# Optimization experiments

Measured on AMD Instinct MI355X. Metric: run time of the kernel, lower is better.

## Reference

```python
import jax, jax.numpy as jnp
import numpy as np

N_NODES = 100000
D_IN = 256
D_OUT = 128
N_EDGES = 1600000


def setup_inputs() -> dict:
    key = jax.random.key(0)
    k1, k2, k3, k4 = jax.random.split(key, 4)
    x = jax.random.normal(k1, (N_NODES, D_IN), dtype=jnp.float32)
    edge_index = jax.random.randint(k2, (2, N_EDGES), 0, N_NODES, dtype=jnp.int64)
    # GCNConv parameters (glorot-style scale)
    W = jax.random.normal(k3, (D_IN, D_OUT), dtype=jnp.float32) * (1.0 / np.sqrt(D_IN))
    b = jax.random.normal(k4, (D_OUT,), dtype=jnp.float32) * 0.01
    return {"x": x, "edge_index": edge_index, "W": W, "b": b}


def reference(x, edge_index, W, b):
    n = x.shape[0]
    # add self-loops (PyG GCNConv default)
    loop = jnp.arange(n, dtype=edge_index.dtype)
    src = jnp.concatenate([edge_index[0], loop])
    dst = jnp.concatenate([edge_index[1], loop])
    # symmetric normalization: deg^-1/2[src] * deg^-1/2[dst]
    ones = jnp.ones(src.shape[0], dtype=x.dtype)
    deg = jax.ops.segment_sum(ones, dst, num_segments=n)
    dinv = jnp.where(deg > 0, jax.lax.rsqrt(deg), 0.0)
    norm = dinv[src] * dinv[dst]  # [E+N]
    # linear transform at nodes, then gather-scale-scatter over edges
    h = x @ W  # [N, d_out]
    msg = h[src] * norm[:, None]  # [E+N, d_out]
    out = jax.ops.segment_sum(msg, dst, num_segments=n) + b
    # CRD.forward: relu then dropout (identity in eval mode)
    return jax.nn.relu(out)
```

## Files before the change

### kernel.cpp

```cpp
#include <hip/hip_runtime.h>
#include <stdint.h>

#define D_IN 256
#define D_OUT 128
#define MAXB 800
#define NCHUNK 256

typedef __attribute__((ext_vector_type(8))) short bf16x8;
typedef __attribute__((ext_vector_type(4))) float f32x4;

__device__ __forceinline__ unsigned short f2bf(float f) {
  union { float f; uint32_t u; } v; v.f = f;
  uint32_t u = v.u;
  uint32_t r = (u + 0x7FFFu + ((u >> 16) & 1u)) >> 16;
  return (unsigned short)r;
}
__device__ __forceinline__ float bf_lo(uint32_t u) {
  union { uint32_t u; float f; } v; v.u = u << 16; return v.f;
}
__device__ __forceinline__ float bf_hi(uint32_t u) {
  union { uint32_t u; float f; } v; v.u = u & 0xFFFF0000u; return v.f;
}
__device__ __forceinline__ f32x4 bq_a(uint4 u) {
  return f32x4{bf_lo(u.x), bf_hi(u.x), bf_lo(u.y), bf_hi(u.y)};
}
__device__ __forceinline__ f32x4 bq_b(uint4 u) {
  return f32x4{bf_lo(u.z), bf_hi(u.z), bf_lo(u.w), bf_hi(u.w)};
}

__device__ __forceinline__ void dma16(const float* gsrc, float* ldst) {
  __builtin_amdgcn_global_load_lds(
      (const __attribute__((address_space(1))) void*)gsrc,
      (__attribute__((address_space(3))) void*)ldst, 16, 0, 0);
}

__global__ __launch_bounds__(256) void k_conv_w(const float* __restrict__ W,
                                                unsigned short* __restrict__ wt) {
  int idx = blockIdx.x * 256 + threadIdx.x;
  int n = idx >> 8;
  int k = idx & 255;
  wt[idx] = f2bf(W[k * D_OUT + n]);
}

__global__ __launch_bounds__(512) void k_gemm(const float* __restrict__ x,
                                              const unsigned short* __restrict__ wt,
                                              const float* __restrict__ dinv,
                                              unsigned short* __restrict__ hp, int N) {
  __shared__ float xl[2][16][256];

  int wave = threadIdx.x >> 6;
  int lane = threadIdx.x & 63;
  int m = lane & 15;
  int q = lane >> 4;

  bf16x8 bw[8];
  const unsigned short* wrow = wt + (size_t)(wave * 16 + m) * D_IN + q * 8;
#pragma unroll
  for (int kt = 0; kt < 8; ++kt)
    bw[kt] = *reinterpret_cast<const bf16x8*>(wrow + kt * 32);

  int tiles = (N + 15) >> 4;
  int ipb = (tiles + gridDim.x - 1) / gridDim.x;
  int t0 = blockIdx.x * ipb;
  int tend = t0 + ipb;
  if (tend > tiles) tend = tiles;
  if (t0 >= tend) return;

  auto stage_tile = [&](int buf, int tt) {
#pragma unroll
    for (int rr = 0; rr < 2; ++rr) {
      int r = wave + rr * 8;
      const float* gsrc = x + ((size_t)tt * 16 + r) * D_IN + ((lane ^ (r & 7)) << 2);
      dma16(gsrc, &xl[buf][r][0]);
    }
  };

  stage_tile(0, t0);
  __syncthreads();

  int cur = 0;
  int sw = m & 7;

  for (int t = t0; t < tend; ++t) {
    if (t + 1 < tend) stage_tile(cur ^ 1, t + 1);

    const float* prow = &xl[cur][m][0];
    f32x4 acc = {0.f, 0.f, 0.f, 0.f};
#pragma unroll
    for (int kt = 0; kt < 8; ++kt) {
      int g0 = q * 2 + kt * 8;
      float4 u0 = *reinterpret_cast<const float4*>(prow + ((g0 ^ sw) << 2));
      float4 u1 = *reinterpret_cast<const float4*>(prow + (((g0 + 1) ^ sw) << 2));
      bf16x8 av;
      av[0] = (short)f2bf(u0.x); av[1] = (short)f2bf(u0.y);
      av[2] = (short)f2bf(u0.z); av[3] = (short)f2bf(u0.w);
      av[4] = (short)f2bf(u1.x); av[5] = (short)f2bf(u1.y);
      av[6] = (short)f2bf(u1.z); av[7] = (short)f2bf(u1.w);
      acc = __builtin_amdgcn_mfma_f32_16x16x32_bf16(av, bw[kt], acc, 0, 0, 0);
    }

    int r0 = t * 16;
#pragma unroll
    for (int r = 0; r < 4; ++r) {
      int row = r0 + q * 4 + r;
      hp[(size_t)row * D_OUT + wave * 16 + m] = f2bf(dinv[row] * acc[r]);
    }

    __syncthreads();
    cur ^= 1;
  }
}

__global__ __launch_bounds__(256) void k_passA(const int* __restrict__ ei, int E, int CH,
                                               int NB, int* __restrict__ cntm) {
  __shared__ int bins[MAXB];
  int c = blockIdx.x;
  for (int b = threadIdx.x; b < NB; b += 256) bins[b] = 0;
  __syncthreads();
  int start = c * CH, end = min(E, start + CH);
  for (int eb = start + (int)threadIdx.x * 4; eb < end; eb += 1024) {
    int kmax = end - eb; if (kmax > 4) kmax = 4;
    if (kmax == 4) {
      int4 v = *reinterpret_cast<const int4*>(ei + E + eb);
      atomicAdd(&bins[v.x >> 7], 1);
      atomicAdd(&bins[v.y >> 7], 1);
      atomicAdd(&bins[v.z >> 7], 1);
      atomicAdd(&bins[v.w >> 7], 1);
    } else {
      for (int k = 0; k < kmax; ++k) atomicAdd(&bins[ei[E + eb + k] >> 7], 1);
    }
  }
  __syncthreads();
  for (int b = threadIdx.x; b < NB; b += 256) cntm[(size_t)b * NCHUNK + c] = bins[b];
}

__global__ __launch_bounds__(NCHUNK) void k_scanB1(const int* __restrict__ cntm,
                                                   int* __restrict__ ofs,
                                                   int* __restrict__ tot) {
  __shared__ int sc[NCHUNK];
  int b = blockIdx.x, t = threadIdx.x;
  int v = cntm[(size_t)b * NCHUNK + t];
  sc[t] = v;
  __syncthreads();
  for (int off = 1; off < NCHUNK; off <<= 1) {
    int val = (t >= off) ? sc[t - off] : 0;
    __syncthreads();
    sc[t] += val;
    __syncthreads();
  }
  ofs[(size_t)b * NCHUNK + t] = sc[t] - v;
  if (t == NCHUNK - 1) tot[b] = sc[t];
}

__global__ __launch_bounds__(256) void k_scanB2(const int* __restrict__ tot,
                                                int* __restrict__ base, int NB,
                                                int* __restrict__ nptr, int N, int E) {
  __shared__ int sc[256];
  int t = threadIdx.x;
  int v[4];
  int s = 0;
#pragma unroll
  for (int j = 0; j < 4; ++j) {
    int i = t * 4 + j;
    v[j] = (i < NB) ? tot[i] : 0;
    s += v[j];
  }
  sc[t] = s;
  __syncthreads();
  for (int off = 1; off < 256; off <<= 1) {
    int val = (t >= off) ? sc[t - off] : 0;
    __syncthreads();
    sc[t] += val;
    __syncthreads();
  }
  int ex = sc[t] - s;
#pragma unroll
  for (int j = 0; j < 4; ++j) {
    int i = t * 4 + j;
    if (i < NB) base[i] = ex;
    ex += v[j];
  }
  if (t == 0) nptr[N] = E;
}

__global__ __launch_bounds__(256) void k_passC(const int* __restrict__ ei, int E, int CH,
                                               int NB, const int* __restrict__ ofs,
                                               const int* __restrict__ base,
                                               int* __restrict__ P) {
  __shared__ int cur[MAXB];
  int c = blockIdx.x;
  for (int b = threadIdx.x; b < NB; b += 256)
    cur[b] = base[b] + ofs[(size_t)b * NCHUNK + c];
  __syncthreads();
  int start = c * CH, end = min(E, start + CH);
  for (int eb = start + (int)threadIdx.x * 4; eb < end; eb += 1024) {
    int kmax = end - eb; if (kmax > 4) kmax = 4;
    int s4[4], d4[4];
    if (kmax == 4) {
      int4 vs = *reinterpret_cast<const int4*>(ei + eb);
      int4 vd = *reinterpret_cast<const int4*>(ei + E + eb);
      s4[0] = vs.x; s4[1] = vs.y; s4[2] = vs.z; s4[3] = vs.w;
      d4[0] = vd.x; d4[1] = vd.y; d4[2] = vd.z; d4[3] = vd.w;
    } else {
      for (int k = 0; k < kmax; ++k) { s4[k] = ei[eb + k]; d4[k] = ei[E + eb + k]; }
    }
#pragma unroll
    for (int k = 0; k < 4; ++k) {
      if (k >= kmax) break;
      int d = d4[k];
      int p = atomicAdd(&cur[d >> 7], 1);
      P[p] = s4[k] | ((d & 127) << 17);
    }
  }
}

__global__ __launch_bounds__(256) void k_sortd(const int* __restrict__ P,
                                               const int* __restrict__ base,
                                               const int* __restrict__ tot,
                                               int* __restrict__ nptr,
                                               float* __restrict__ dinv,
                                               int* __restrict__ P2, int N) {
  __shared__ int ideg[128];
  __shared__ int sc[128];
  __shared__ int cur[128];
  int b = blockIdx.x, t = threadIdx.x;
  if (t < 128) ideg[t] = 0;
  __syncthreads();
  int s0 = base[b], T = tot[b];
  for (int i = s0 + t; i < s0 + T; i += 256) atomicAdd(&ideg[P[i] >> 17], 1);
  __syncthreads();
  if (t < 128) sc[t] = ideg[t];
  __syncthreads();
  for (int off = 1; off < 128; off <<= 1) {
    int v = (t < 128 && t >= off) ? sc[t - off] : 0;
    __syncthreads();
    if (t < 128) sc[t] += v;
    __syncthreads();
  }
  if (t < 128) {
    int exc = s0 + sc[t] - ideg[t];
    int node = b * 128 + t;
    if (node < N) {
      nptr[node] = exc;
      dinv[node] = rsqrtf(1.0f + (float)ideg[t]);
    }
    cur[t] = exc;
  }
  __syncthreads();
  for (int i = s0 + t; i < s0 + T; i += 256) {
    int pk = P[i];
    int p = atomicAdd(&cur[pk >> 17], 1);
    P2[p] = pk & 0x1FFFF;
  }
}

__global__ __launch_bounds__(256) void k_agg(const int* __restrict__ P2,
                                             const int* __restrict__ nptr,
                                             const uint4* __restrict__ hrows,
                                             const float* __restrict__ dinv,
                                             const float* __restrict__ bias,
                                             float* __restrict__ out, int N) {
  int wave = threadIdx.x >> 6, lane = threadIdx.x & 63;
  int node = blockIdx.x * 4 + wave;
  if (node >= N) return;
  int rs = nptr[node], re = nptr[node + 1];
  int j = lane >> 4, c = lane & 15;

  f32x4 acc0 = {0.f, 0.f, 0.f, 0.f};
  f32x4 acc1 = {0.f, 0.f, 0.f, 0.f};

  int e = rs + j;
  for (; e + 12 < re; e += 16) {
    int s0 = P2[e];
    int s1 = P2[e + 4];
    int s2 = P2[e + 8];
    int s3 = P2[e + 12];
    uint4 u0 = hrows[(size_t)s0 * 16 + c];
    uint4 u1 = hrows[(size_t)s1 * 16 + c];
    uint4 u2 = hrows[(size_t)s2 * 16 + c];
    uint4 u3 = hrows[(size_t)s3 * 16 + c];
    acc0 += bq_a(u0); acc1 += bq_b(u0);
    acc0 += bq_a(u1); acc1 += bq_b(u1);
    acc0 += bq_a(u2); acc1 += bq_b(u2);
    acc0 += bq_a(u3); acc1 += bq_b(u3);
  }
  for (; e < re; e += 4) {
    int s0 = P2[e];
    uint4 u0 = hrows[(size_t)s0 * 16 + c];
    acc0 += bq_a(u0); acc1 += bq_b(u0);
  }

  float acc[8] = {acc0[0], acc0[1], acc0[2], acc0[3],
                  acc1[0], acc1[1], acc1[2], acc1[3]};
#pragma unroll
  for (int k = 0; k < 8; ++k) {
    acc[k] += __shfl_xor(acc[k], 16);
    acc[k] += __shfl_xor(acc[k], 32);
  }
  if (j == 0) {
    float rsn = dinv[node];
    uint4 uh = hrows[(size_t)node * 16 + c];
    float self[8] = {bf_lo(uh.x), bf_hi(uh.x), bf_lo(uh.y), bf_hi(uh.y),
                     bf_lo(uh.z), bf_hi(uh.z), bf_lo(uh.w), bf_hi(uh.w)};
    const float4* b4 = reinterpret_cast<const float4*>(bias);
    float4 b0 = b4[c * 2], b1 = b4[c * 2 + 1];
    float bb[8] = {b0.x, b0.y, b0.z, b0.w, b1.x, b1.y, b1.z, b1.w};
    float o[8];
#pragma unroll
    for (int k = 0; k < 8; ++k) {
      float v = rsn * (acc[k] + self[k]) + bb[k];
      o[k] = v > 0.f ? v : 0.f;
    }
    float4* orow = reinterpret_cast<float4*>(out + (size_t)node * D_OUT + c * 8);
    orow[0] = float4{o[0], o[1], o[2], o[3]};
    orow[1] = float4{o[4], o[5], o[6], o[7]};
  }
}

extern "C" void kernel_launch(void* const* d_in, const int* in_sizes, int n_in,
                              void* d_out, int out_size, void* d_ws, size_t ws_size,
                              hipStream_t stream) {
  const float* x = (const float*)d_in[0];
  const int* ei = (const int*)d_in[1];
  const float* W = (const float*)d_in[2];
  const float* bias = (const float*)d_in[3];
  int N = in_sizes[0] / D_IN;
  int E = in_sizes[1] / 2;
  float* out = (float*)d_out;

  int NB = (N + 127) >> 7;
  int CH = ((E + NCHUNK - 1) / NCHUNK + 3) & ~3;

  char* w = (char*)d_ws;
  size_t off = 0;
  auto alloc = [&](size_t bytes) -> void* {
    void* p = w + off;
    off = (off + bytes + 255) & ~(size_t)255;
    return p;
  };
  unsigned short* wt = (unsigned short*)alloc((size_t)D_IN * D_OUT * 2);
  unsigned short* hp = (unsigned short*)alloc((size_t)N * D_OUT * 2);
  float* dinv = (float*)alloc((size_t)N * 4);
  int* cntm = (int*)alloc((size_t)NB * NCHUNK * 4);
  int* ofs = (int*)alloc((size_t)NB * NCHUNK * 4);
  int* tot = (int*)alloc((size_t)NB * 4);
  int* base = (int*)alloc((size_t)NB * 4);
  int* nptr = (int*)alloc((size_t)(N + 1) * 4);
  int* P = (int*)alloc((size_t)E * 4);
  int* P2 = (int*)alloc((size_t)E * 4);
  (void)ws_size; (void)n_in; (void)out_size;

  int tiles = (N + 15) >> 4;
  int gblocks = tiles < 1024 ? tiles : 1024;

  k_conv_w<<<(D_IN * D_OUT) / 256, 256, 0, stream>>>(W, wt);
  k_passA<<<NCHUNK, 256, 0, stream>>>(ei, E, CH, NB, cntm);
  k_scanB1<<<NB, NCHUNK, 0, stream>>>(cntm, ofs, tot);
  k_scanB2<<<1, 256, 0, stream>>>(tot, base, NB, nptr, N, E);
  k_passC<<<NCHUNK, 256, 0, stream>>>(ei, E, CH, NB, ofs, base, P);
  k_sortd<<<NB, 256, 0, stream>>>(P, base, tot, nptr, dinv, P2, N);
  k_gemm<<<gblocks, 512, 0, stream>>>(x, wt, dinv, hp, N);
  k_agg<<<(N + 3) / 4, 256, 0, stream>>>(P2, nptr, (const uint4*)hp, dinv, bias, out, N);
}
```

Measured before the change: 299.6 us.

## Split projected features into column planes and aggregate per feature slice

The GEMM now writes h as eight column planes of 16 bf16 features per node instead of row-major 128-wide rows. The aggregation kernel is relaunched with eight blocks per node group, each block gathering only one 32-byte slice per edge, so each plane's working set is much smaller and can better fit in cache. The cost is that the CSR indices and row pointers are read eight times, and each gather is a smaller, less efficient access.

```diff
diff --git a/kernel.cpp b/kernel.cpp
--- a/kernel.cpp
+++ b/kernel.cpp
@@ -80,6 +80,7 @@
 
   int cur = 0;
   int sw = m & 7;
+  unsigned short* hpw = hp + (size_t)wave * N * 16;
 
   for (int t = t0; t < tend; ++t) {
     if (t + 1 < tend) stage_tile(cur ^ 1, t + 1);
@@ -103,7 +104,7 @@
 #pragma unroll
     for (int r = 0; r < 4; ++r) {
       int row = r0 + q * 4 + r;
-      hp[(size_t)row * D_OUT + wave * 16 + m] = f2bf(dinv[row] * acc[r]);
+      hpw[(size_t)row * 16 + m] = f2bf(dinv[row] * acc[r]);
     }
 
     __syncthreads();
@@ -256,54 +257,47 @@
 
 __global__ __launch_bounds__(256) void k_agg(const int* __restrict__ P2,
                                              const int* __restrict__ nptr,
-                                             const uint4* __restrict__ hrows,
+                                             const uint4* __restrict__ hpq,
                                              const float* __restrict__ dinv,
                                              const float* __restrict__ bias,
                                              float* __restrict__ out, int N) {
   int wave = threadIdx.x >> 6, lane = threadIdx.x & 63;
-  int node = blockIdx.x * 4 + wave;
-  if (node >= N) return;
-  int rs = nptr[node], re = nptr[node + 1];
-  int j = lane >> 4, c = lane & 15;
+  int s = blockIdx.x & 7;
+  int g = blockIdx.x >> 3;
+  int nsub = lane >> 4;
+  int j = (lane >> 1) & 7;
+  int c = lane & 1;
+  int node = g * 16 + wave * 4 + nsub;
+  const uint4* plane = hpq + (size_t)s * N * 2;
 
   f32x4 acc0 = {0.f, 0.f, 0.f, 0.f};
   f32x4 acc1 = {0.f, 0.f, 0.f, 0.f};
-
-  int e = rs + j;
-  for (; e + 12 < re; e += 16) {
-    int s0 = P2[e];
-    int s1 = P2[e + 4];
-    int s2 = P2[e + 8];
-    int s3 = P2[e + 12];
-    uint4 u0 = hrows[(size_t)s0 * 16 + c];
-    uint4 u1 = hrows[(size_t)s1 * 16 + c];
-    uint4 u2 = hrows[(size_t)s2 * 16 + c];
-    uint4 u3 = hrows[(size_t)s3 * 16 + c];
-    acc0 += bq_a(u0); acc1 += bq_b(u0);
-    acc0 += bq_a(u1); acc1 += bq_b(u1);
-    acc0 += bq_a(u2); acc1 += bq_b(u2);
-    acc0 += bq_a(u3); acc1 += bq_b(u3);
-  }
-  for (; e < re; e += 4) {
-    int s0 = P2[e];
-    uint4 u0 = hrows[(size_t)s0 * 16 + c];
-    acc0 += bq_a(u0); acc1 += bq_b(u0);
+  int rs = 0, re = 0;
+  if (node < N) { rs = nptr[node]; re = nptr[node + 1]; }
+
+  for (int e = rs + j; e < re; e += 8) {
+    int src = P2[e];
+    uint4 u = plane[(size_t)src * 2 + c];
+    acc0 += bq_a(u);
+    acc1 += bq_b(u);
   }
 
   float acc[8] = {acc0[0], acc0[1], acc0[2], acc0[3],
                   acc1[0], acc1[1], acc1[2], acc1[3]};
 #pragma unroll
   for (int k = 0; k < 8; ++k) {
-    acc[k] += __shfl_xor(acc[k], 16);
-    acc[k] += __shfl_xor(acc[k], 32);
-  }
-  if (j == 0) {
+    acc[k] += __shfl_xor(acc[k], 2);
+    acc[k] += __shfl_xor(acc[k], 4);
+    acc[k] += __shfl_xor(acc[k], 8);
+  }
+  if (j == 0 && node < N) {
     float rsn = dinv[node];
-    uint4 uh = hrows[(size_t)node * 16 + c];
+    uint4 uh = plane[(size_t)node * 2 + c];
     float self[8] = {bf_lo(uh.x), bf_hi(uh.x), bf_lo(uh.y), bf_hi(uh.y),
                      bf_lo(uh.z), bf_hi(uh.z), bf_lo(uh.w), bf_hi(uh.w)};
+    int gi = s * 2 + c;
     const float4* b4 = reinterpret_cast<const float4*>(bias);
-    float4 b0 = b4[c * 2], b1 = b4[c * 2 + 1];
+    float4 b0 = b4[gi * 2], b1 = b4[gi * 2 + 1];
     float bb[8] = {b0.x, b0.y, b0.z, b0.w, b1.x, b1.y, b1.z, b1.w};
     float o[8];
 #pragma unroll
@@ -311,7 +305,7 @@
       float v = rsn * (acc[k] + self[k]) + bb[k];
       o[k] = v > 0.f ? v : 0.f;
     }
-    float4* orow = reinterpret_cast<float4*>(out + (size_t)node * D_OUT + c * 8);
+    float4* orow = reinterpret_cast<float4*>(out + (size_t)node * D_OUT + gi * 8);
     orow[0] = float4{o[0], o[1], o[2], o[3]};
     orow[1] = float4{o[4], o[5], o[6], o[7]};
   }
@@ -360,5 +354,6 @@
   k_passC<<<NCHUNK, 256, 0, stream>>>(ei, E, CH, NB, ofs, base, P);
   k_sortd<<<NB, 256, 0, stream>>>(P, base, tot, nptr, dinv, P2, N);
   k_gemm<<<gblocks, 512, 0, stream>>>(x, wt, dinv, hp, N);
-  k_agg<<<(N + 3) / 4, 256, 0, stream>>>(P2, nptr, (const uint4*)hp, dinv, bias, out, N);
-}
+  int gn = (N + 15) / 16;
+  k_agg<<<gn * 8, 256, 0, stream>>>(P2, nptr, (const uint4*)hp, dinv, bias, out, N);
+}
```

Result: slower. 334.3 us (+11.6%).
